# Performance work log

Hardware: AMD Instinct MI355X
Metric: run time of the kernel (lower is better)

Reference implementation:

```python
import jax, jax.numpy as jnp
import numpy as np

DIM0, DIMO, WIDTH, DEPTH = 64, 16, 128, 6  # depth = number of weight matrices
N = 524288


def setup_inputs() -> dict:
    key = jax.random.key(0)
    ks = jax.random.split(key, DEPTH + 1)
    x = jax.random.normal(ks[0], (N, DIM0), dtype=jnp.float32)
    bd0 = 1.0 / np.sqrt(DIM0)   # first layer init bound (per torch code)
    bd = 1.0 / np.sqrt(WIDTH)   # remaining layers init bound
    W0 = jax.random.uniform(ks[1], (DIM0, WIDTH), minval=-bd0, maxval=bd0, dtype=jnp.float32)
    W1 = jax.random.uniform(ks[2], (WIDTH, WIDTH), minval=-bd, maxval=bd, dtype=jnp.float32)
    W2 = jax.random.uniform(ks[3], (WIDTH, WIDTH), minval=-bd, maxval=bd, dtype=jnp.float32)
    W3 = jax.random.uniform(ks[4], (WIDTH, WIDTH), minval=-bd, maxval=bd, dtype=jnp.float32)
    W4 = jax.random.uniform(ks[5], (WIDTH, WIDTH), minval=-bd, maxval=bd, dtype=jnp.float32)
    W5 = jax.random.uniform(ks[6], (WIDTH, DIMO), minval=-bd, maxval=bd, dtype=jnp.float32)
    bias = jnp.zeros((DIMO,), dtype=jnp.float32)
    return {"x": x, "W0": W0, "W1": W1, "W2": W2, "W3": W3, "W4": W4, "W5": W5, "bias": bias}


def reference(x, W0, W1, W2, W3, W4, W5, bias):
    # Fully-fused MLP math: matmul (no bias) + ReLU for every layer except the
    # last (output_activation='None'); then cast back to x dtype and add bias.
    h = jax.nn.relu(x @ W0)
    h = jax.nn.relu(h @ W1)
    h = jax.nn.relu(h @ W2)
    h = jax.nn.relu(h @ W3)
    h = jax.nn.relu(h @ W4)
    out = (h @ W5).astype(x.dtype) + bias
    return out
```

## Files before the change

### kernel.cpp

```cpp
#include <hip/hip_runtime.h>
#include <stdint.h>


typedef __bf16 bf16x8 __attribute__((ext_vector_type(8)));
typedef __bf16 bf16x4 __attribute__((ext_vector_type(4)));
typedef float  floatx4 __attribute__((ext_vector_type(4)));

#define GAS __attribute__((address_space(1)))
#define LAS __attribute__((address_space(3)))

constexpr int NS   = 524288;
constexpr int TILE = 128;
constexpr int NBLK = NS / TILE;

constexpr int WTOT = 9472;

__global__ void prep_weights(const float* __restrict__ W0, const float* __restrict__ W1,
                             const float* __restrict__ W2, const float* __restrict__ W3,
                             const float* __restrict__ W4, const float* __restrict__ W5,
                             bf16x8* __restrict__ ws) {
  int gid = blockIdx.x * blockDim.x + threadIdx.x;
  if (gid >= WTOT) return;
  const float* Wsrc; int nout, cpr, base;
  if (gid < 1024)      { Wsrc = W0; nout = 128; cpr = 8;  base = 0;    }
  else if (gid < 3072) { Wsrc = W1; nout = 128; cpr = 16; base = 1024; }
  else if (gid < 5120) { Wsrc = W2; nout = 128; cpr = 16; base = 3072; }
  else if (gid < 7168) { Wsrc = W3; nout = 128; cpr = 16; base = 5120; }
  else if (gid < 9216) { Wsrc = W4; nout = 128; cpr = 16; base = 7168; }
  else                 { Wsrc = W5; nout = 16;  cpr = 16; base = 9216; }
  int id = gid - base;
  int n  = id / cpr;
  int p  = id % cpr;
  int c  = p ^ (n & 7);
  bf16x8 v;
#pragma unroll
  for (int j = 0; j < 8; ++j)
    v[j] = (__bf16)Wsrc[(8 * c + j) * nout + n];
  ws[gid] = v;
}

__device__ __forceinline__ void stage_w(const bf16x8* __restrict__ src, bf16x8* dst,
                                        int nchunks, int w, int lane) {
  int per  = nchunks >> 2;
  int base = w * per;
  for (int i = 0; i < per; i += 64) {
    __builtin_amdgcn_global_load_lds(
        (const GAS void*)(src + base + i + lane),
        (LAS void*)(dst + base + i),
        16, 0, 0);
  }
}

__device__ __forceinline__ void zero_acc(floatx4 acc[4][4]) {
  floatx4 z = {0.f, 0.f, 0.f, 0.f};
#pragma unroll
  for (int i = 0; i < 4; ++i)
#pragma unroll
    for (int j = 0; j < 4; ++j) acc[i][j] = z;
}

template <int KT, int CPR>
__device__ __forceinline__ void layer_mm(const bf16x8* Wb, const bf16x8* Hb,
                                         floatx4 acc[4][4], int m_base, int n_base,
                                         int l15, int g) {
#pragma unroll
  for (int kt = 0; kt < KT; ++kt) {
    const int cx = (kt * 4 + g) ^ (l15 & 7);
    bf16x8 a[4], b[4];
#pragma unroll
    for (int i = 0; i < 4; ++i) a[i] = Wb[(m_base + 16 * i + l15) * CPR + cx];
#pragma unroll
    for (int i = 0; i < 4; ++i) b[i] = Hb[(n_base + 16 * i + l15) * 16 + cx];
#pragma unroll
    for (int ot = 0; ot < 4; ++ot)
#pragma unroll
      for (int nt = 0; nt < 4; ++nt)
        acc[ot][nt] = __builtin_amdgcn_mfma_f32_16x16x32_bf16(a[ot], b[nt], acc[ot][nt], 0, 0, 0);
  }
}

__device__ __forceinline__ void write_h(bf16x4* H8, const floatx4 acc[4][4],
                                        int m_base, int n_base, int l15, int g) {
#pragma unroll
  for (int ot = 0; ot < 4; ++ot) {
    int ob    = m_base + 16 * ot + 4 * g;
    int phys8 = (((ob >> 3) ^ (l15 & 7)) << 1) | ((ob >> 2) & 1);
#pragma unroll
    for (int nt = 0; nt < 4; ++nt) {
      int s = n_base + 16 * nt + l15;
      floatx4 v = acc[ot][nt];
      bf16x4 h;
      h[0] = (__bf16)fmaxf(v[0], 0.0f);
      h[1] = (__bf16)fmaxf(v[1], 0.0f);
      h[2] = (__bf16)fmaxf(v[2], 0.0f);
      h[3] = (__bf16)fmaxf(v[3], 0.0f);
      H8[s * 32 + phys8] = h;
    }
  }
}

__global__ void __launch_bounds__(256) mlp_kernel(const float* __restrict__ x,
                                                  const float* __restrict__ bias,
                                                  const bf16x8* __restrict__ wimg,
                                                  float* __restrict__ out) {
  __shared__ bf16x8 Hbuf[TILE * 16];
  __shared__ bf16x8 Wbuf[2048];

  const int t    = threadIdx.x;
  const int lane = t & 63;
  const int w    = t >> 6;
  const int l15  = lane & 15;
  const int g    = lane >> 4;
  const int m_base = (w & 1) * 64;
  const int n_base = (w >> 1) * 64;
  const int tile = blockIdx.x;

  constexpr int WOFF[6] = {0, 1024, 3072, 5120, 7168, 9216};
  constexpr int WCNT[6] = {1024, 2048, 2048, 2048, 2048, 256};

  stage_w(wimg + WOFF[0], Wbuf, WCNT[0], w, lane);

  const float* xt = x + (size_t)tile * TILE * 64;
#pragma unroll
  for (int i = 0; i < 4; ++i) {
    int f2 = t + 256 * i;
    int s = f2 >> 3, c = f2 & 7;
    const floatx4* src = (const floatx4*)(xt + f2 * 8);
    floatx4 lo = src[0], hi = src[1];
    bf16x8 v;
    v[0] = (__bf16)lo[0]; v[1] = (__bf16)lo[1]; v[2] = (__bf16)lo[2]; v[3] = (__bf16)lo[3];
    v[4] = (__bf16)hi[0]; v[5] = (__bf16)hi[1]; v[6] = (__bf16)hi[2]; v[7] = (__bf16)hi[3];
    Hbuf[s * 16 + (c ^ (s & 7))] = v;
  }
  __syncthreads();

  floatx4 acc[4][4];

  zero_acc(acc);
  layer_mm<2, 8>(Wbuf, Hbuf, acc, m_base, n_base, l15, g);
  __syncthreads();
  stage_w(wimg + WOFF[1], Wbuf, WCNT[1], w, lane);
  write_h((bf16x4*)Hbuf, acc, m_base, n_base, l15, g);
  __syncthreads();

#pragma unroll
  for (int l = 1; l <= 4; ++l) {
    zero_acc(acc);
    layer_mm<4, 16>(Wbuf, Hbuf, acc, m_base, n_base, l15, g);
    __syncthreads();
    stage_w(wimg + WOFF[l + 1], Wbuf, WCNT[l + 1], w, lane);
    write_h((bf16x4*)Hbuf, acc, m_base, n_base, l15, g);
    __syncthreads();
  }

  floatx4 a5[2];
  {
    floatx4 z = {0.f, 0.f, 0.f, 0.f};
    a5[0] = z; a5[1] = z;
  }
  const int n5 = w * 32;
#pragma unroll
  for (int kt = 0; kt < 4; ++kt) {
    int cx = (kt * 4 + g) ^ (l15 & 7);
    bf16x8 a = Wbuf[l15 * 16 + cx];
#pragma unroll
    for (int nt = 0; nt < 2; ++nt) {
      bf16x8 b = Hbuf[(n5 + 16 * nt + l15) * 16 + cx];
      a5[nt] = __builtin_amdgcn_mfma_f32_16x16x32_bf16(a, b, a5[nt], 0, 0, 0);
    }
  }
  floatx4 bv = *(const floatx4*)(bias + 4 * g);
  floatx4* outv = (floatx4*)out;
#pragma unroll
  for (int nt = 0; nt < 2; ++nt) {
    int s = tile * TILE + n5 + 16 * nt + l15;
    outv[s * 4 + g] = a5[nt] + bv;
  }
}

extern "C" void kernel_launch(void* const* d_in, const int* in_sizes, int n_in,
                              void* d_out, int out_size, void* d_ws, size_t ws_size,
                              hipStream_t stream) {
  (void)in_sizes; (void)n_in; (void)out_size; (void)ws_size;
  const float* x    = (const float*)d_in[0];
  const float* W0   = (const float*)d_in[1];
  const float* W1   = (const float*)d_in[2];
  const float* W2   = (const float*)d_in[3];
  const float* W3   = (const float*)d_in[4];
  const float* W4   = (const float*)d_in[5];
  const float* W5   = (const float*)d_in[6];
  const float* bias = (const float*)d_in[7];
  bf16x8* ws = (bf16x8*)d_ws;

  prep_weights<<<(WTOT + 255) / 256, 256, 0, stream>>>(W0, W1, W2, W3, W4, W5, ws);
  mlp_kernel<<<NBLK, 256, 0, stream>>>(x, bias, (const bf16x8*)ws, (float*)d_out);
}
```

Baseline: 268.2 us.

## Read MLP weights directly from global memory and halve the sample tile

Weights are no longer staged into LDS with global_load_lds. Each wave now loads its MFMA A-fragments straight from the global bf16 weight image, so the prep kernel drops the XOR swizzle for weights. The tile shrinks to 64 samples with 128 threads per block, each wave owning 64 output rows, and launch bounds request 5 blocks per CU to raise occupancy and cut LDS use. The trade-off is that every block re-reads all weights through the cache hierarchy each layer, with global-load latency inside the MFMA loop and no prefetch.

```diff
diff --git a/kernel.cpp b/kernel.cpp
--- a/kernel.cpp
+++ b/kernel.cpp
@@ -6,11 +6,8 @@
 typedef __bf16 bf16x4 __attribute__((ext_vector_type(4)));
 typedef float  floatx4 __attribute__((ext_vector_type(4)));
 
-#define GAS __attribute__((address_space(1)))
-#define LAS __attribute__((address_space(3)))
-
 constexpr int NS   = 524288;
-constexpr int TILE = 128;
+constexpr int TILE = 64;
 constexpr int NBLK = NS / TILE;
 
 constexpr int WTOT = 9472;
@@ -30,25 +27,12 @@
   else                 { Wsrc = W5; nout = 16;  cpr = 16; base = 9216; }
   int id = gid - base;
   int n  = id / cpr;
-  int p  = id % cpr;
-  int c  = p ^ (n & 7);
+  int c  = id % cpr;
   bf16x8 v;
 #pragma unroll
   for (int j = 0; j < 8; ++j)
     v[j] = (__bf16)Wsrc[(8 * c + j) * nout + n];
   ws[gid] = v;
-}
-
-__device__ __forceinline__ void stage_w(const bf16x8* __restrict__ src, bf16x8* dst,
-                                        int nchunks, int w, int lane) {
-  int per  = nchunks >> 2;
-  int base = w * per;
-  for (int i = 0; i < per; i += 64) {
-    __builtin_amdgcn_global_load_lds(
-        (const GAS void*)(src + base + i + lane),
-        (LAS void*)(dst + base + i),
-        16, 0, 0);
-  }
 }
 
 __device__ __forceinline__ void zero_acc(floatx4 acc[4][4]) {
@@ -60,17 +44,17 @@
 }
 
 template <int KT, int CPR>
-__device__ __forceinline__ void layer_mm(const bf16x8* Wb, const bf16x8* Hb,
-                                         floatx4 acc[4][4], int m_base, int n_base,
-                                         int l15, int g) {
+__device__ __forceinline__ void layer_mm(const bf16x8* __restrict__ Wg, const bf16x8* Hb,
+                                         floatx4 acc[4][4], int m_base, int l15, int g) {
 #pragma unroll
   for (int kt = 0; kt < KT; ++kt) {
-    const int cx = (kt * 4 + g) ^ (l15 & 7);
+    const int cw = kt * 4 + g;
+    const int cx = cw ^ (l15 & 7);
     bf16x8 a[4], b[4];
 #pragma unroll
-    for (int i = 0; i < 4; ++i) a[i] = Wb[(m_base + 16 * i + l15) * CPR + cx];
+    for (int i = 0; i < 4; ++i) a[i] = Wg[(m_base + 16 * i + l15) * CPR + cw];
 #pragma unroll
-    for (int i = 0; i < 4; ++i) b[i] = Hb[(n_base + 16 * i + l15) * 16 + cx];
+    for (int i = 0; i < 4; ++i) b[i] = Hb[(16 * i + l15) * 16 + cx];
 #pragma unroll
     for (int ot = 0; ot < 4; ++ot)
 #pragma unroll
@@ -80,14 +64,14 @@
 }
 
 __device__ __forceinline__ void write_h(bf16x4* H8, const floatx4 acc[4][4],
-                                        int m_base, int n_base, int l15, int g) {
+                                        int m_base, int l15, int g) {
 #pragma unroll
   for (int ot = 0; ot < 4; ++ot) {
     int ob    = m_base + 16 * ot + 4 * g;
     int phys8 = (((ob >> 3) ^ (l15 & 7)) << 1) | ((ob >> 2) & 1);
 #pragma unroll
     for (int nt = 0; nt < 4; ++nt) {
-      int s = n_base + 16 * nt + l15;
+      int s = 16 * nt + l15;
       floatx4 v = acc[ot][nt];
       bf16x4 h;
       h[0] = (__bf16)fmaxf(v[0], 0.0f);
@@ -99,31 +83,26 @@
   }
 }
 
-__global__ void __launch_bounds__(256) mlp_kernel(const float* __restrict__ x,
-                                                  const float* __restrict__ bias,
-                                                  const bf16x8* __restrict__ wimg,
-                                                  float* __restrict__ out) {
+__global__ void __launch_bounds__(128, 5) mlp_kernel(const float* __restrict__ x,
+                                                     const float* __restrict__ bias,
+                                                     const bf16x8* __restrict__ wimg,
+                                                     float* __restrict__ out) {
   __shared__ bf16x8 Hbuf[TILE * 16];
-  __shared__ bf16x8 Wbuf[2048];
 
   const int t    = threadIdx.x;
   const int lane = t & 63;
   const int w    = t >> 6;
   const int l15  = lane & 15;
   const int g    = lane >> 4;
-  const int m_base = (w & 1) * 64;
-  const int n_base = (w >> 1) * 64;
+  const int m_base = w * 64;
   const int tile = blockIdx.x;
 
   constexpr int WOFF[6] = {0, 1024, 3072, 5120, 7168, 9216};
-  constexpr int WCNT[6] = {1024, 2048, 2048, 2048, 2048, 256};
-
-  stage_w(wimg + WOFF[0], Wbuf, WCNT[0], w, lane);
 
   const float* xt = x + (size_t)tile * TILE * 64;
 #pragma unroll
   for (int i = 0; i < 4; ++i) {
-    int f2 = t + 256 * i;
+    int f2 = t + 128 * i;
     int s = f2 >> 3, c = f2 & 7;
     const floatx4* src = (const floatx4*)(xt + f2 * 8);
     floatx4 lo = src[0], hi = src[1];
@@ -137,22 +116,21 @@
   floatx4 acc[4][4];
 
   zero_acc(acc);
-  layer_mm<2, 8>(Wbuf, Hbuf, acc, m_base, n_base, l15, g);
+  layer_mm<2, 8>(wimg + WOFF[0], Hbuf, acc, m_base, l15, g);
   __syncthreads();
-  stage_w(wimg + WOFF[1], Wbuf, WCNT[1], w, lane);
-  write_h((bf16x4*)Hbuf, acc, m_base, n_base, l15, g);
+  write_h((bf16x4*)Hbuf, acc, m_base, l15, g);
   __syncthreads();
 
 #pragma unroll
   for (int l = 1; l <= 4; ++l) {
     zero_acc(acc);
-    layer_mm<4, 16>(Wbuf, Hbuf, acc, m_base, n_base, l15, g);
+    layer_mm<4, 16>(wimg + WOFF[l], Hbuf, acc, m_base, l15, g);
     __syncthreads();
-    stage_w(wimg + WOFF[l + 1], Wbuf, WCNT[l + 1], w, lane);
-    write_h((bf16x4*)Hbuf, acc, m_base, n_base, l15, g);
+    write_h((bf16x4*)Hbuf, acc, m_base, l15, g);
     __syncthreads();
   }
 
+  const bf16x8* W5g = wimg + WOFF[5];
   floatx4 a5[2];
   {
     floatx4 z = {0.f, 0.f, 0.f, 0.f};
@@ -161,8 +139,9 @@
   const int n5 = w * 32;
 #pragma unroll
   for (int kt = 0; kt < 4; ++kt) {
-    int cx = (kt * 4 + g) ^ (l15 & 7);
-    bf16x8 a = Wbuf[l15 * 16 + cx];
+    int cw = kt * 4 + g;
+    int cx = cw ^ (l15 & 7);
+    bf16x8 a = W5g[l15 * 16 + cw];
 #pragma unroll
     for (int nt = 0; nt < 2; ++nt) {
       bf16x8 b = Hbuf[(n5 + 16 * nt + l15) * 16 + cx];
@@ -193,5 +172,5 @@
   bf16x8* ws = (bf16x8*)d_ws;
 
   prep_weights<<<(WTOT + 255) / 256, 256, 0, stream>>>(W0, W1, W2, W3, W4, W5, ws);
-  mlp_kernel<<<NBLK, 256, 0, stream>>>(x, bias, (const bf16x8*)ws, (float*)d_out);
+  mlp_kernel<<<NBLK, 128, 0, stream>>>(x, bias, (const bf16x8*)ws, (float*)d_out);
 }
```

Measured after the change: 422.0 us. 1.57x slower.
